# Performance work log

Hardware: AMD Instinct MI355X
Metric: run time of the kernel (lower is better)

The kernel has to match this reference:

```python
import jax, jax.numpy as jnp
import numpy as np

NH = 16   # num heads
CS = 16   # inner chunk size

def _gelu(x):
    return jax.nn.gelu(x, approximate=True)

def _diff_gelu(x):
    t = jnp.tanh(0.79788456 * x * (1.0 + 0.044715 * x * x))
    return 0.5 * x * ((1.0 - t * t) * (0.79788456 + 0.1070322243 * x * x)) + 0.5 * (1.0 + t)

def _ln_fused_l2_bwd(x, tgt, gamma, beta, eps=1e-6):
    # x, tgt: [B*nh, CS, f]; gamma/beta: [1, nh, 1, f]
    Bnh, N, HF = x.shape
    mu = x.mean(-1, keepdims=True)
    var = x.var(-1, keepdims=True)
    std = jnp.sqrt(var + eps)
    x_hat = (x - mu) / std
    y = gamma * x_hat.reshape(-1, NH, N, HF) + beta
    go = y - tgt.reshape(-1, NH, N, HF)
    gxh = (go * gamma).reshape(Bnh, N, HF)
    return (HF * gxh - gxh.sum(-1, keepdims=True) - x_hat * (gxh * x_hat).sum(-1, keepdims=True)) / (HF * std)

def setup_inputs() -> dict:
    key = jax.random.key(0)
    ks = jax.random.split(key, 8)
    B, nh, f, hf4, n_chunks = 4, NH, 64, 256, 128
    Bnh = B * nh
    XQ = jax.random.normal(ks[0], (n_chunks, Bnh, CS, f), jnp.float32)
    XK = jax.random.normal(ks[1], (n_chunks, Bnh, CS, f), jnp.float32)
    XV = jax.random.normal(ks[2], (n_chunks, Bnh, CS, f), jnp.float32)
    # inner-loop lr coeffs (ilr * token_idx ~ lr/head_dim): small positive
    coeff = jax.random.uniform(ks[3], (n_chunks, Bnh, CS, 1), jnp.float32) * 0.01
    coeff_last = jax.random.uniform(ks[4], (n_chunks, Bnh, 1, 1), jnp.float32) * 0.01
    W1 = jax.random.normal(ks[5], (Bnh, f, hf4), jnp.float32) * 0.02
    b1 = jnp.zeros((Bnh, 1, hf4), jnp.float32)
    W2 = jax.random.normal(ks[6], (Bnh, hf4, f), jnp.float32) * 0.02
    b2 = jnp.zeros((Bnh, 1, f), jnp.float32)
    ln_weight = jnp.ones((1, nh, 1, f), jnp.float32)
    ln_bias = jnp.zeros((1, nh, 1, f), jnp.float32)
    return dict(XQ=XQ, XK=XK, XV=XV, coeff=coeff, coeff_last=coeff_last,
                W1=W1, b1=b1, W2=W2, b2=b2, ln_weight=ln_weight, ln_bias=ln_bias)

def reference(XQ, XK, XV, coeff, coeff_last, W1, b1, W2, b2, ln_weight, ln_bias):
    n_chunks, Bnh, _, f = XQ.shape
    attn_b = jnp.tril(jnp.ones((CS, CS), XQ.dtype))

    def step(carry, inp):
        W1c, b1c, W2c, b2c = carry
        xv, xk, xq, c, cl = inp
        Z1 = xk @ W1c + b1c                      # [Bnh, CS, 4f]
        X2 = _gelu(Z1)
        Z2 = X2 @ W2c + b2c                      # [Bnh, CS, f]
        dZ2 = _ln_fused_l2_bwd(Z2, xv - xk, ln_weight, ln_bias)
        dZ1 = (dZ2 @ W2c.transpose(0, 2, 1)) * _diff_gelu(Z1)
        b1_bar = b1c - c * (attn_b @ dZ1)
        A1 = jnp.tril(xq @ xk.transpose(0, 2, 1))
        Z1_bar = xq @ W1c - c * (A1 @ dZ1) + b1_bar
        X2_bar = _gelu(Z1_bar)
        b2_bar = b2c - c * (attn_b @ dZ2)
        A2 = jnp.tril(X2_bar @ X2.transpose(0, 2, 1))
        Z2_bar = X2_bar @ W2c - c * (A2 @ dZ2) + b2_bar
        W1n = W1c - cl * (xk.transpose(0, 2, 1) @ dZ1)
        W2n = W2c - cl * (X2.transpose(0, 2, 1) @ dZ2)
        return (W1n, b1_bar[:, -1:], W2n, b2_bar[:, -1:]), Z2_bar

    _, Z2_all = jax.lax.scan(step, (W1, b1, W2, b2), (XV, XK, XQ, coeff, coeff_last))
    # [n_chunks, Bnh, CS, f] -> [Bnh, N, f]
    return Z2_all.transpose(1, 0, 2, 3).reshape(Bnh, n_chunks * CS, f)
```

## Files before the change

kernel.cpp:

```cpp
#include <hip/hip_runtime.h>

typedef __attribute__((ext_vector_type(8))) short bf16x8;
typedef __attribute__((ext_vector_type(4))) float f32x4;
typedef __attribute__((ext_vector_type(2))) unsigned int u32x2;

#define MFMA16(a,b,c) __builtin_amdgcn_mfma_f32_16x16x32_bf16(a,b,c,0,0,0)
#define A_GELU 0.7978845608028654f

#define OFF_W1B   0u
#define OFF_W2F   36864u
#define OFF_XK    70656u
#define OFF_XQ    72960u
#define OFF_X2    75264u
#define OFF_X2B   83712u
#define OFF_DZ2B  92160u
#define OFF_DZ1CT 94464u
#define OFF_DZ2CT 114944u
#define OFF_M1    120064u
#define OFF_M2    121344u
#define OFF_Z2F   122624u
#define OFF_Z2G   126976u
#define OFF_TGT   131328u
#define OFF_B2    135424u
#define OFF_COEF  135936u
#define OFF_CL    136000u
#define SMEM_BYTES 136016u

__device__ __forceinline__ float fast_tanh(float u){
    float e = __expf(2.0f*u);
    return 1.0f - 2.0f/(e + 1.0f);
}
__device__ __forceinline__ float gelu_f(float x){
    float t = fast_tanh(A_GELU*(x + 0.044715f*x*x*x));
    return 0.5f*x*(1.0f+t);
}
__device__ __forceinline__ float dgelu_f(float x){
    float x2 = x*x;
    float t = fast_tanh(A_GELU*x*(1.0f + 0.044715f*x2));
    return 0.5f*x*((1.0f-t*t)*(A_GELU + 0.1070322243f*x2)) + 0.5f*(1.0f+t);
}
__device__ __forceinline__ short f2bf(float f){
    unsigned u = __builtin_bit_cast(unsigned, f);
    u += 0x7FFFu + ((u >> 16) & 1u);
    return (short)(u >> 16);
}
__device__ __forceinline__ float bf2f(unsigned short s){
    unsigned u = ((unsigned)s) << 16;
    return __builtin_bit_cast(float, u);
}
__device__ __forceinline__ unsigned pkbf(float a, float b){
    unsigned r;
    asm("v_cvt_pk_bf16_f32 %0, %1, %2" : "=v"(r) : "v"(a), "v"(b));
    return r;
}
__device__ __forceinline__ bf16x8 ldfrag(const unsigned short* p){
    return *(const bf16x8*)p;
}

__global__ __launch_bounds__(512, 1)
void ttt_m2(const float* __restrict__ XQ, const float* __restrict__ XK,
            const float* __restrict__ XV, const float* __restrict__ coeff,
            const float* __restrict__ coeff_last,
            const float* __restrict__ W1g, const float* __restrict__ b1g,
            const float* __restrict__ W2g, const float* __restrict__ b2g,
            const float* __restrict__ gammag, const float* __restrict__ betag,
            float* __restrict__ out)
{
    const int h  = blockIdx.x;
    const int t  = threadIdx.x;
    const int l  = t & 63;
    const int w  = t >> 6;
    const int lo = l & 15;
    const int hi = l >> 4;

    extern __shared__ char smem[];
    unsigned short* sW1bu  = (unsigned short*)(smem + OFF_W1B);
    unsigned short* sW2fu  = (unsigned short*)(smem + OFF_W2F);
    unsigned short* sxku   = (unsigned short*)(smem + OFF_XK);
    unsigned short* sxqu   = (unsigned short*)(smem + OFF_XQ);
    unsigned short* sX2u   = (unsigned short*)(smem + OFF_X2);
    unsigned short* sX2bu  = (unsigned short*)(smem + OFF_X2B);
    unsigned short* sdZ2bu = (unsigned short*)(smem + OFF_DZ2B);
    unsigned short* sdZ1ct = (unsigned short*)(smem + OFF_DZ1CT);
    unsigned short* sdZ2ct = (unsigned short*)(smem + OFF_DZ2CT);
    unsigned short* sM1u   = (unsigned short*)(smem + OFF_M1);
    unsigned short* sM2u   = (unsigned short*)(smem + OFF_M2);
    float* sZ2f  = (float*)(smem + OFF_Z2F);
    float* sZ2g  = (float*)(smem + OFF_Z2G);
    float* stgt  = (float*)(smem + OFF_TGT);
    float* b2f   = (float*)(smem + OFF_B2);
    float* scoef = (float*)(smem + OFF_COEF);
    float* sCL   = (float*)(smem + OFF_CL);

    const int base1 = h*16384;
    const int base2 = h*16384;

    float mW1[4][2][4];
    float mW2[2][4][4];
    #pragma unroll
    for (int mt = 0; mt < 4; ++mt)
      #pragma unroll
      for (int tix = 0; tix < 2; ++tix)
        #pragma unroll
        for (int reg = 0; reg < 4; ++reg) {
            const int m = mt*16 + hi*4 + reg, n = (2*w + tix)*16 + lo;
            mW1[mt][tix][reg] = W1g[base1 + m*256 + n];
        }
    #pragma unroll
    for (int mi = 0; mi < 2; ++mi)
      #pragma unroll
      for (int nt = 0; nt < 4; ++nt)
        #pragma unroll
        for (int reg = 0; reg < 4; ++reg) {
            const int m = (2*w + mi)*16 + hi*4 + reg, n = nt*16 + lo;
            mW2[mi][nt][reg] = W2g[base2 + m*64 + n];
        }
    float b1reg[2];
    b1reg[0] = b1g[h*256 + (2*w)*16 + lo];
    b1reg[1] = b1g[h*256 + (2*w+1)*16 + lo];

    for (int i = 0; i < 32; ++i) {
        const int idx = i*512 + t;
        const int m = idx >> 8, n = idx & 255;
        sW1bu[n*72 + m] = f2bf(W1g[base1 + idx]);
    }
    for (int i = 0; i < 32; ++i) {
        const int idx = i*512 + t;
        const int hf = idx >> 6, f = idx & 63;
        sW2fu[f*264 + hf] = f2bf(W2g[base2 + idx]);
    }
    if (t < 64) b2f[t] = b2g[h*64 + t];
    if (t < 256) {
        for (int k = 16; k < 40; ++k) sdZ1ct[t*40 + k] = 0;
    }
    if (t < 64) {
        for (int k = 16; k < 40; ++k) sdZ2ct[t*40 + k] = 0;
    }
    if (t < 16) {
        for (int k = 16; k < 40; ++k) { sM1u[t*40 + k] = 0; sM2u[t*40 + k] = 0; }
    }

    const float gj = gammag[(h & 15)*64 + l];
    const float bj = betag [(h & 15)*64 + l];

    {
        const int r0 = w*2;
        const float xk0 = XK[h*1024 + r0*64 + l],     xq0 = XQ[h*1024 + r0*64 + l];
        const float xk1 = XK[h*1024 + (r0+1)*64 + l], xq1 = XQ[h*1024 + (r0+1)*64 + l];
        const float xv0 = XV[h*1024 + r0*64 + l],     xv1 = XV[h*1024 + (r0+1)*64 + l];
        const unsigned pkk = pkbf(xk0, xk1), pkq = pkbf(xq0, xq1);
        sxku[r0*72 + l]     = (unsigned short)pkk;
        sxku[(r0+1)*72 + l] = (unsigned short)(pkk >> 16);
        sxqu[r0*72 + l]     = (unsigned short)pkq;
        sxqu[(r0+1)*72 + l] = (unsigned short)(pkq >> 16);
        stgt[r0*64 + l]     = xv0 - xk0;
        stgt[(r0+1)*64 + l] = xv1 - xk1;
        if (t < 16)  scoef[t] = coeff[h*16 + t];
        if (t == 16) sCL[0]   = coeff_last[h];
    }
    __syncthreads();

    for (int ci = 0; ci < 128; ++ci) {
        const float clv = sCL[0];
        const float c15 = scoef[15];
        float crs[4];
        #pragma unroll
        for (int reg = 0; reg < 4; ++reg) crs[reg] = scoef[hi*4 + reg];

        float pxk[4], pxq[4], pxv[4];
        float pcf = 0.f, pcl = 0.f;
        if (w >= 4 && ci < 127) {
            const int cb1 = (ci + 1)*65536 + h*1024;
            const int r0 = (w - 4)*4;
            #pragma unroll
            for (int i = 0; i < 4; ++i) {
                pxk[i] = XK[cb1 + (r0 + i)*64 + l];
                pxq[i] = XQ[cb1 + (r0 + i)*64 + l];
                pxv[i] = XV[cb1 + (r0 + i)*64 + l];
            }
            const int u = t - 256;
            if (u < 16)  pcf = coeff[(ci + 1)*1024 + h*16 + u];
            if (u == 16) pcl = coeff_last[(ci + 1)*64 + h];
        }

        float z1s[8];
        bf16x8 afk0 = ldfrag(sxku + lo*72 + hi*8);
        bf16x8 afk1 = ldfrag(sxku + lo*72 + 32 + hi*8);
        #pragma unroll
        for (int tix = 0; tix < 2; ++tix) {
            const int n = (2*w + tix)*16 + lo;
            f32x4 acc = {b1reg[tix], b1reg[tix], b1reg[tix], b1reg[tix]};
            acc = MFMA16(afk0, ldfrag(sW1bu + n*72 + hi*8), acc);
            acc = MFMA16(afk1, ldfrag(sW1bu + n*72 + 32 + hi*8), acc);
            float g[4];
            #pragma unroll
            for (int reg = 0; reg < 4; ++reg) {
                z1s[tix*4 + reg] = acc[reg];
                g[reg] = gelu_f(acc[reg]);
            }
            const unsigned p01 = pkbf(g[0], g[1]), p23 = pkbf(g[2], g[3]);
            sX2u[(hi*4+0)*264 + n] = (unsigned short)p01;
            sX2u[(hi*4+1)*264 + n] = (unsigned short)(p01 >> 16);
            sX2u[(hi*4+2)*264 + n] = (unsigned short)p23;
            sX2u[(hi*4+3)*264 + n] = (unsigned short)(p23 >> 16);
        }
        if (w == 0) {
            bf16x8 aq0 = ldfrag(sxqu + lo*72 + hi*8);
            bf16x8 aq1 = ldfrag(sxqu + lo*72 + 32 + hi*8);
            f32x4 a1 = {0.f, 0.f, 0.f, 0.f};
            a1 = MFMA16(aq0, afk0, a1);
            a1 = MFMA16(aq1, afk1, a1);
            #pragma unroll
            for (int reg = 0; reg < 4; ++reg) {
                const int r = hi*4 + reg;
                const float v = (lo <= r) ? (-crs[reg]*(a1[reg] + 1.0f)) : 0.0f;
                sM1u[r*40 + lo] = f2bf(v);
            }
        }
        #pragma unroll
        for (int mi = 0; mi < 2; ++mi)
          #pragma unroll
          for (int nt = 0; nt < 4; ++nt) {
                const int n = nt*16 + lo, m0 = (2*w + mi)*16 + hi*4;
                *(u32x2*)&sW2fu[n*264 + m0] =
                    (u32x2){pkbf(mW2[mi][nt][0], mW2[mi][nt][1]),
                            pkbf(mW2[mi][nt][2], mW2[mi][nt][3])};
          }
        __syncthreads();

        const int tile = w & 3, kh = w >> 2;
        const int nf = tile*16 + lo;
        {
            f32x4 acc;
            if (kh == 0) {
                const float b2v = b2f[(ci & 1)*64 + nf];
                acc = (f32x4){b2v, b2v, b2v, b2v};
            } else acc = (f32x4){0.f, 0.f, 0.f, 0.f};
            #pragma unroll
            for (int s = 0; s < 4; ++s) {
                const int k = (kh*4 + s)*32 + hi*8;
                acc = MFMA16(ldfrag(sX2u + lo*264 + k),
                             ldfrag(sW2fu + nf*264 + k), acc);
            }
            float* dst = (kh == 0) ? sZ2g : sZ2f;
            #pragma unroll
            for (int reg = 0; reg < 4; ++reg)
                dst[(hi*4 + reg)*68 + nf] = acc[reg];
        }
        __syncthreads();

        {
            float dzp[2];
            #pragma unroll
            for (int i = 0; i < 2; ++i) {
                const int r = w*2 + i;
                const float z2 = sZ2f[r*68 + l] + sZ2g[r*68 + l];
                float s1 = z2, s2 = z2*z2;
                #pragma unroll
                for (int m = 1; m < 64; m <<= 1) { s1 += __shfl_xor(s1, m); s2 += __shfl_xor(s2, m); }
                const float mu   = s1*(1.0f/64.0f);
                const float var  = s2*(1.0f/64.0f) - mu*mu;
                const float rstd = rsqrtf(var + 1e-6f);
                const float xh   = (z2 - mu)*rstd;
                const float go   = gj*xh + bj - stgt[r*64 + l];
                const float gg   = go*gj;
                float u1 = gg, u2 = gg*xh;
                #pragma unroll
                for (int m = 1; m < 64; m <<= 1) { u1 += __shfl_xor(u1, m); u2 += __shfl_xor(u2, m); }
                dzp[i] = (64.0f*gg - u1 - xh*u2)*(rstd*(1.0f/64.0f));
            }
            const unsigned pk = pkbf(dzp[0], dzp[1]);
            sdZ2bu[(w*2)*72 + l]   = (unsigned short)pk;
            sdZ2bu[(w*2+1)*72 + l] = (unsigned short)(pk >> 16);
            *(unsigned*)&sdZ2ct[l*40 + w*2] = pk;
        }
        __syncthreads();

        float b1old[2];
        {
            bf16x8 ad0 = ldfrag(sdZ2bu + lo*72 + hi*8);
            bf16x8 ad1 = ldfrag(sdZ2bu + lo*72 + 32 + hi*8);
            #pragma unroll
            for (int tix = 0; tix < 2; ++tix) {
                const int n = (2*w + tix)*16 + lo;
                f32x4 acc = {0.f, 0.f, 0.f, 0.f};
                bf16x8 bw;
                #pragma unroll
                for (int j = 0; j < 8; ++j) bw[j] = (short)sW2fu[(hi*8 + j)*264 + n];
                acc = MFMA16(ad0, bw, acc);
                #pragma unroll
                for (int j = 0; j < 8; ++j) bw[j] = (short)sW2fu[(32 + hi*8 + j)*264 + n];
                acc = MFMA16(ad1, bw, acc);
                float dv[4], cs = 0.f;
                #pragma unroll
                for (int reg = 0; reg < 4; ++reg) {
                    dv[reg] = acc[reg]*dgelu_f(z1s[tix*4 + reg]);
                    cs += dv[reg];
                }
                *(u32x2*)&sdZ1ct[n*40 + hi*4] =
                    (u32x2){pkbf(dv[0], dv[1]), pkbf(dv[2], dv[3])};
                cs += __shfl_xor(cs, 16);
                cs += __shfl_xor(cs, 32);
                b1old[tix] = b1reg[tix];
                b1reg[tix] -= c15*cs;
            }
        }
        __syncthreads();

        {
            bf16x8 aq0 = ldfrag(sxqu + lo*72 + hi*8);
            bf16x8 aq1 = ldfrag(sxqu + lo*72 + 32 + hi*8);
            bf16x8 am1 = ldfrag(sM1u + lo*40 + hi*8);
            #pragma unroll
            for (int tix = 0; tix < 2; ++tix) {
                const int n = (2*w + tix)*16 + lo;
                f32x4 acc = {b1old[tix], b1old[tix], b1old[tix], b1old[tix]};
                acc = MFMA16(aq0, ldfrag(sW1bu + n*72 + hi*8), acc);
                acc = MFMA16(aq1, ldfrag(sW1bu + n*72 + 32 + hi*8), acc);
                acc = MFMA16(am1, ldfrag(sdZ1ct + n*40 + hi*8), acc);
                float g[4];
                #pragma unroll
                for (int reg = 0; reg < 4; ++reg) g[reg] = gelu_f(acc[reg]);
                const unsigned p01 = pkbf(g[0], g[1]), p23 = pkbf(g[2], g[3]);
                sX2bu[(hi*4+0)*264 + n] = (unsigned short)p01;
                sX2bu[(hi*4+1)*264 + n] = (unsigned short)(p01 >> 16);
                sX2bu[(hi*4+2)*264 + n] = (unsigned short)p23;
                sX2bu[(hi*4+3)*264 + n] = (unsigned short)(p23 >> 16);
            }
            bf16x8 bz0 = ldfrag(sdZ1ct + ((2*w)*16 + lo)*40 + hi*8);
            bf16x8 bz1 = ldfrag(sdZ1ct + ((2*w+1)*16 + lo)*40 + hi*8);
            #pragma unroll
            for (int mt = 0; mt < 4; ++mt) {
                bf16x8 axt = (bf16x8){0,0,0,0,0,0,0,0};
                if (l < 32) {
                    #pragma unroll
                    for (int j = 0; j < 8; ++j)
                        axt[j] = (short)sxku[(hi*8 + j)*72 + (mt*16 + lo)];
                }
                f32x4 z4 = {0.f,0.f,0.f,0.f};
                f32x4 u0 = MFMA16(axt, bz0, z4);
                f32x4 u1 = MFMA16(axt, bz1, z4);
                #pragma unroll
                for (int reg = 0; reg < 4; ++reg) {
                    mW1[mt][0][reg] -= clv*u0[reg];
                    mW1[mt][1][reg] -= clv*u1[reg];
                }
            }
        }
        __syncthreads();

        {
            bf16x8 bz2[4];
            #pragma unroll
            for (int nt = 0; nt < 4; ++nt)
                bz2[nt] = ldfrag(sdZ2ct + (nt*16 + lo)*40 + hi*8);
            #pragma unroll
            for (int mi = 0; mi < 2; ++mi) {
                const int mt = 2*w + mi;
                bf16x8 ax2 = (bf16x8){0,0,0,0,0,0,0,0};
                if (l < 32) {
                    #pragma unroll
                    for (int j = 0; j < 8; ++j)
                        ax2[j] = (short)sX2u[(hi*8 + j)*264 + (mt*16 + lo)];
                }
                #pragma unroll
                for (int nt = 0; nt < 4; ++nt) {
                    f32x4 z4 = {0.f,0.f,0.f,0.f};
                    f32x4 u = MFMA16(ax2, bz2[nt], z4);
                    #pragma unroll
                    for (int reg = 0; reg < 4; ++reg)
                        mW2[mi][nt][reg] -= clv*u[reg];
                }
            }
            if (w == 0) {
                f32x4 a2 = {0.f,0.f,0.f,0.f};
                #pragma unroll
                for (int ks = 0; ks < 8; ++ks) {
                    const int k = ks*32 + hi*8;
                    a2 = MFMA16(ldfrag(sX2bu + lo*264 + k),
                                ldfrag(sX2u + lo*264 + k), a2);
                }
                #pragma unroll
                for (int reg = 0; reg < 4; ++reg) {
                    const int r = hi*4 + reg;
                    const float v = (lo <= r) ? (-crs[reg]*(a2[reg] + 1.0f)) : 0.0f;
                    sM2u[r*40 + lo] = f2bf(v);
                }
            }
            if (w == 1) {
                float cs = 0.f;
                #pragma unroll
                for (int k = 0; k < 16; ++k) cs += bf2f(sdZ2ct[l*40 + k]);
                b2f[((ci + 1) & 1)*64 + l] = b2f[(ci & 1)*64 + l] - c15*cs;
            }
            #pragma unroll
            for (int mt = 0; mt < 4; ++mt)
              #pragma unroll
              for (int tix = 0; tix < 2; ++tix) {
                    const int n = (2*w + tix)*16 + lo, m0 = mt*16 + hi*4;
                    *(u32x2*)&sW1bu[n*72 + m0] =
                        (u32x2){pkbf(mW1[mt][tix][0], mW1[mt][tix][1]),
                                pkbf(mW1[mt][tix][2], mW1[mt][tix][3])};
              }
        }
        __syncthreads();

        if (w < 4) {
            const int nf2 = w*16 + lo;
            const float b2v = b2f[(ci & 1)*64 + nf2];
            f32x4 acc = {b2v, b2v, b2v, b2v};
            #pragma unroll
            for (int s = 0; s < 8; ++s) {
                const int k0 = s*32 + hi*8;
                acc = MFMA16(ldfrag(sX2bu + lo*264 + k0),
                             ldfrag(sW2fu + nf2*264 + k0), acc);
            }
            acc = MFMA16(ldfrag(sM2u + lo*40 + hi*8),
                         ldfrag(sdZ2ct + nf2*40 + hi*8), acc);
            #pragma unroll
            for (int reg = 0; reg < 4; ++reg)
                out[h*131072 + (ci*16 + hi*4 + reg)*64 + nf2] = acc[reg];
        } else if (ci < 127) {
            const int r0 = (w - 4)*4;
            #pragma unroll
            for (int p = 0; p < 2; ++p) {
                const int r = r0 + 2*p;
                const unsigned pkk = pkbf(pxk[2*p], pxk[2*p+1]);
                const unsigned pkq = pkbf(pxq[2*p], pxq[2*p+1]);
                sxku[r*72 + l]     = (unsigned short)pkk;
                sxku[(r+1)*72 + l] = (unsigned short)(pkk >> 16);
                sxqu[r*72 + l]     = (unsigned short)pkq;
                sxqu[(r+1)*72 + l] = (unsigned short)(pkq >> 16);
                stgt[r*64 + l]     = pxv[2*p]   - pxk[2*p];
                stgt[(r+1)*64 + l] = pxv[2*p+1] - pxk[2*p+1];
            }
            const int u = t - 256;
            if (u < 16)  scoef[u] = pcf;
            if (u == 16) sCL[0]   = pcl;
        }
        __syncthreads();
    }
}

extern "C" void kernel_launch(void* const* d_in, const int* in_sizes, int n_in,
                              void* d_out, int out_size, void* d_ws, size_t ws_size,
                              hipStream_t stream) {
    const float* XQ  = (const float*)d_in[0];
    const float* XK  = (const float*)d_in[1];
    const float* XV  = (const float*)d_in[2];
    const float* cf  = (const float*)d_in[3];
    const float* cfl = (const float*)d_in[4];
    const float* W1  = (const float*)d_in[5];
    const float* b1  = (const float*)d_in[6];
    const float* W2  = (const float*)d_in[7];
    const float* b2  = (const float*)d_in[8];
    const float* gam = (const float*)d_in[9];
    const float* bet = (const float*)d_in[10];
    float* o = (float*)d_out;

    hipFuncSetAttribute((const void*)ttt_m2,
                        hipFuncAttributeMaxDynamicSharedMemorySize, SMEM_BYTES);
    ttt_m2<<<64, 512, SMEM_BYTES, stream>>>(XQ, XK, XV, cf, cfl, W1, b1, W2, b2, gam, bet, o);
}
```

Before: 976.4 us.

## Add transposed W2 and XK LDS copies, shrink padded K-pad buffers

Keeps a second, transposed bf16 copy of W2 and of XK in shared memory so MFMA operand fragments come from one vector load each instead of eight strided scalar gathers. The K=16 buffers (dZ1, dZ2, M1, M2) now use a 24-element stride, and a masked fragment load zero-fills the upper K half instead of relying on zeroed padding. The target (XV-XK) is stored as bf16. The b2 column sum now reads from the row-major dZ2 buffer. Each step pays extra LDS writes to keep the transposed W2 copy current, and shared memory use grows, and the bf16 target loses precision in the LayerNorm gradient.

```diff
diff --git a/kernel.cpp b/kernel.cpp
--- a/kernel.cpp
+++ b/kernel.cpp
@@ -9,22 +9,24 @@
 
 #define OFF_W1B   0u
 #define OFF_W2F   36864u
-#define OFF_XK    70656u
-#define OFF_XQ    72960u
-#define OFF_X2    75264u
-#define OFF_X2B   83712u
-#define OFF_DZ2B  92160u
-#define OFF_DZ1CT 94464u
-#define OFF_DZ2CT 114944u
-#define OFF_M1    120064u
-#define OFF_M2    121344u
-#define OFF_Z2F   122624u
-#define OFF_Z2G   126976u
-#define OFF_TGT   131328u
-#define OFF_B2    135424u
-#define OFF_COEF  135936u
-#define OFF_CL    136000u
-#define SMEM_BYTES 136016u
+#define OFF_W2T   70656u
+#define OFF_XK    107520u
+#define OFF_XQ    109824u
+#define OFF_XKT   112128u
+#define OFF_X2    115200u
+#define OFF_X2B   123648u
+#define OFF_DZ2B  132096u
+#define OFF_DZ1CT 134400u
+#define OFF_DZ2CT 146688u
+#define OFF_M1    149760u
+#define OFF_M2    150528u
+#define OFF_Z2F   151296u
+#define OFF_Z2G   155520u
+#define OFF_TGT   159744u
+#define OFF_B2    162048u
+#define OFF_COEF  162560u
+#define OFF_CL    162624u
+#define SMEM_BYTES 162640u
 
 __device__ __forceinline__ float fast_tanh(float u){
     float e = __expf(2.0f*u);
@@ -55,6 +57,11 @@
 }
 __device__ __forceinline__ bf16x8 ldfrag(const unsigned short* p){
     return *(const bf16x8*)p;
+}
+__device__ __forceinline__ bf16x8 ldmask16(const unsigned short* row, int hi){
+    bf16x8 r = {0,0,0,0,0,0,0,0};
+    if (hi < 2) r = *(const bf16x8*)(row + hi*8);
+    return r;
 }
 
 __global__ __launch_bounds__(512, 1)
@@ -76,8 +83,10 @@
     extern __shared__ char smem[];
     unsigned short* sW1bu  = (unsigned short*)(smem + OFF_W1B);
     unsigned short* sW2fu  = (unsigned short*)(smem + OFF_W2F);
+    unsigned short* sW2T   = (unsigned short*)(smem + OFF_W2T);
     unsigned short* sxku   = (unsigned short*)(smem + OFF_XK);
     unsigned short* sxqu   = (unsigned short*)(smem + OFF_XQ);
+    unsigned short* sxkT   = (unsigned short*)(smem + OFF_XKT);
     unsigned short* sX2u   = (unsigned short*)(smem + OFF_X2);
     unsigned short* sX2bu  = (unsigned short*)(smem + OFF_X2B);
     unsigned short* sdZ2bu = (unsigned short*)(smem + OFF_DZ2B);
@@ -87,7 +96,7 @@
     unsigned short* sM2u   = (unsigned short*)(smem + OFF_M2);
     float* sZ2f  = (float*)(smem + OFF_Z2F);
     float* sZ2g  = (float*)(smem + OFF_Z2G);
-    float* stgt  = (float*)(smem + OFF_TGT);
+    unsigned short* stgtu = (unsigned short*)(smem + OFF_TGT);
     float* b2f   = (float*)(smem + OFF_B2);
     float* scoef = (float*)(smem + OFF_COEF);
     float* sCL   = (float*)(smem + OFF_CL);
@@ -127,18 +136,11 @@
     for (int i = 0; i < 32; ++i) {
         const int idx = i*512 + t;
         const int hf = idx >> 6, f = idx & 63;
-        sW2fu[f*264 + hf] = f2bf(W2g[base2 + idx]);
+        const short v = f2bf(W2g[base2 + idx]);
+        sW2fu[f*264 + hf] = v;
+        sW2T[hf*72 + f]   = v;
     }
     if (t < 64) b2f[t] = b2g[h*64 + t];
-    if (t < 256) {
-        for (int k = 16; k < 40; ++k) sdZ1ct[t*40 + k] = 0;
-    }
-    if (t < 64) {
-        for (int k = 16; k < 40; ++k) sdZ2ct[t*40 + k] = 0;
-    }
-    if (t < 16) {
-        for (int k = 16; k < 40; ++k) { sM1u[t*40 + k] = 0; sM2u[t*40 + k] = 0; }
-    }
 
     const float gj = gammag[(h & 15)*64 + l];
     const float bj = betag [(h & 15)*64 + l];
@@ -149,12 +151,14 @@
         const float xk1 = XK[h*1024 + (r0+1)*64 + l], xq1 = XQ[h*1024 + (r0+1)*64 + l];
         const float xv0 = XV[h*1024 + r0*64 + l],     xv1 = XV[h*1024 + (r0+1)*64 + l];
         const unsigned pkk = pkbf(xk0, xk1), pkq = pkbf(xq0, xq1);
+        const unsigned pkt = pkbf(xv0 - xk0, xv1 - xk1);
         sxku[r0*72 + l]     = (unsigned short)pkk;
         sxku[(r0+1)*72 + l] = (unsigned short)(pkk >> 16);
         sxqu[r0*72 + l]     = (unsigned short)pkq;
         sxqu[(r0+1)*72 + l] = (unsigned short)(pkq >> 16);
-        stgt[r0*64 + l]     = xv0 - xk0;
-        stgt[(r0+1)*64 + l] = xv1 - xk1;
+        *(unsigned*)&sxkT[l*24 + r0] = pkk;
+        stgtu[r0*72 + l]     = (unsigned short)pkt;
+        stgtu[(r0+1)*72 + l] = (unsigned short)(pkt >> 16);
         if (t < 16)  scoef[t] = coeff[h*16 + t];
         if (t == 16) sCL[0]   = coeff_last[h];
     }
@@ -214,7 +218,7 @@
             for (int reg = 0; reg < 4; ++reg) {
                 const int r = hi*4 + reg;
                 const float v = (lo <= r) ? (-crs[reg]*(a1[reg] + 1.0f)) : 0.0f;
-                sM1u[r*40 + lo] = f2bf(v);
+                sM1u[r*24 + lo] = f2bf(v);
             }
         }
         #pragma unroll
@@ -222,9 +226,13 @@
           #pragma unroll
           for (int nt = 0; nt < 4; ++nt) {
                 const int n = nt*16 + lo, m0 = (2*w + mi)*16 + hi*4;
-                *(u32x2*)&sW2fu[n*264 + m0] =
-                    (u32x2){pkbf(mW2[mi][nt][0], mW2[mi][nt][1]),
-                            pkbf(mW2[mi][nt][2], mW2[mi][nt][3])};
+                const unsigned p01 = pkbf(mW2[mi][nt][0], mW2[mi][nt][1]);
+                const unsigned p23 = pkbf(mW2[mi][nt][2], mW2[mi][nt][3]);
+                *(u32x2*)&sW2fu[n*264 + m0] = (u32x2){p01, p23};
+                sW2T[(m0+0)*72 + n] = (unsigned short)p01;
+                sW2T[(m0+1)*72 + n] = (unsigned short)(p01 >> 16);
+                sW2T[(m0+2)*72 + n] = (unsigned short)p23;
+                sW2T[(m0+3)*72 + n] = (unsigned short)(p23 >> 16);
           }
         __syncthreads();
 
@@ -245,7 +253,7 @@
             float* dst = (kh == 0) ? sZ2g : sZ2f;
             #pragma unroll
             for (int reg = 0; reg < 4; ++reg)
-                dst[(hi*4 + reg)*68 + nf] = acc[reg];
+                dst[(hi*4 + reg)*66 + nf] = acc[reg];
         }
         __syncthreads();
 
@@ -254,7 +262,7 @@
             #pragma unroll
             for (int i = 0; i < 2; ++i) {
                 const int r = w*2 + i;
-                const float z2 = sZ2f[r*68 + l] + sZ2g[r*68 + l];
+                const float z2 = sZ2f[r*66 + l] + sZ2g[r*66 + l];
                 float s1 = z2, s2 = z2*z2;
                 #pragma unroll
                 for (int m = 1; m < 64; m <<= 1) { s1 += __shfl_xor(s1, m); s2 += __shfl_xor(s2, m); }
@@ -262,7 +270,7 @@
                 const float var  = s2*(1.0f/64.0f) - mu*mu;
                 const float rstd = rsqrtf(var + 1e-6f);
                 const float xh   = (z2 - mu)*rstd;
-                const float go   = gj*xh + bj - stgt[r*64 + l];
+                const float go   = gj*xh + bj - bf2f(stgtu[r*72 + l]);
                 const float gg   = go*gj;
                 float u1 = gg, u2 = gg*xh;
                 #pragma unroll
@@ -272,7 +280,7 @@
             const unsigned pk = pkbf(dzp[0], dzp[1]);
             sdZ2bu[(w*2)*72 + l]   = (unsigned short)pk;
             sdZ2bu[(w*2+1)*72 + l] = (unsigned short)(pk >> 16);
-            *(unsigned*)&sdZ2ct[l*40 + w*2] = pk;
+            *(unsigned*)&sdZ2ct[l*24 + w*2] = pk;
         }
         __syncthreads();
 
@@ -284,20 +292,15 @@
             for (int tix = 0; tix < 2; ++tix) {
                 const int n = (2*w + tix)*16 + lo;
                 f32x4 acc = {0.f, 0.f, 0.f, 0.f};
-                bf16x8 bw;
-                #pragma unroll
-                for (int j = 0; j < 8; ++j) bw[j] = (short)sW2fu[(hi*8 + j)*264 + n];
-                acc = MFMA16(ad0, bw, acc);
-                #pragma unroll
-                for (int j = 0; j < 8; ++j) bw[j] = (short)sW2fu[(32 + hi*8 + j)*264 + n];
-                acc = MFMA16(ad1, bw, acc);
+                acc = MFMA16(ad0, ldfrag(sW2T + n*72 + hi*8), acc);
+                acc = MFMA16(ad1, ldfrag(sW2T + n*72 + 32 + hi*8), acc);
                 float dv[4], cs = 0.f;
                 #pragma unroll
                 for (int reg = 0; reg < 4; ++reg) {
                     dv[reg] = acc[reg]*dgelu_f(z1s[tix*4 + reg]);
                     cs += dv[reg];
                 }
-                *(u32x2*)&sdZ1ct[n*40 + hi*4] =
+                *(u32x2*)&sdZ1ct[n*24 + hi*4] =
                     (u32x2){pkbf(dv[0], dv[1]), pkbf(dv[2], dv[3])};
                 cs += __shfl_xor(cs, 16);
                 cs += __shfl_xor(cs, 32);
@@ -310,14 +313,14 @@
         {
             bf16x8 aq0 = ldfrag(sxqu + lo*72 + hi*8);
             bf16x8 aq1 = ldfrag(sxqu + lo*72 + 32 + hi*8);
-            bf16x8 am1 = ldfrag(sM1u + lo*40 + hi*8);
+            bf16x8 am1 = ldmask16(sM1u + lo*24, hi);
             #pragma unroll
             for (int tix = 0; tix < 2; ++tix) {
                 const int n = (2*w + tix)*16 + lo;
                 f32x4 acc = {b1old[tix], b1old[tix], b1old[tix], b1old[tix]};
                 acc = MFMA16(aq0, ldfrag(sW1bu + n*72 + hi*8), acc);
                 acc = MFMA16(aq1, ldfrag(sW1bu + n*72 + 32 + hi*8), acc);
-                acc = MFMA16(am1, ldfrag(sdZ1ct + n*40 + hi*8), acc);
+                acc = MFMA16(am1, ldmask16(sdZ1ct + n*24, hi), acc);
                 float g[4];
                 #pragma unroll
                 for (int reg = 0; reg < 4; ++reg) g[reg] = gelu_f(acc[reg]);
@@ -327,16 +330,11 @@
                 sX2bu[(hi*4+2)*264 + n] = (unsigned short)p23;
                 sX2bu[(hi*4+3)*264 + n] = (unsigned short)(p23 >> 16);
             }
-            bf16x8 bz0 = ldfrag(sdZ1ct + ((2*w)*16 + lo)*40 + hi*8);
-            bf16x8 bz1 = ldfrag(sdZ1ct + ((2*w+1)*16 + lo)*40 + hi*8);
+            bf16x8 bz0 = ldmask16(sdZ1ct + ((2*w)*16 + lo)*24, hi);
+            bf16x8 bz1 = ldmask16(sdZ1ct + ((2*w+1)*16 + lo)*24, hi);
             #pragma unroll
             for (int mt = 0; mt < 4; ++mt) {
-                bf16x8 axt = (bf16x8){0,0,0,0,0,0,0,0};
-                if (l < 32) {
-                    #pragma unroll
-                    for (int j = 0; j < 8; ++j)
-                        axt[j] = (short)sxku[(hi*8 + j)*72 + (mt*16 + lo)];
-                }
+                bf16x8 axt = ldmask16(sxkT + (mt*16 + lo)*24, hi);
                 f32x4 z4 = {0.f,0.f,0.f,0.f};
                 f32x4 u0 = MFMA16(axt, bz0, z4);
                 f32x4 u1 = MFMA16(axt, bz1, z4);
@@ -353,7 +351,7 @@
             bf16x8 bz2[4];
             #pragma unroll
             for (int nt = 0; nt < 4; ++nt)
-                bz2[nt] = ldfrag(sdZ2ct + (nt*16 + lo)*40 + hi*8);
+                bz2[nt] = ldmask16(sdZ2ct + (nt*16 + lo)*24, hi);
             #pragma unroll
             for (int mi = 0; mi < 2; ++mi) {
                 const int mt = 2*w + mi;
@@ -384,13 +382,13 @@
                 for (int reg = 0; reg < 4; ++reg) {
                     const int r = hi*4 + reg;
                     const float v = (lo <= r) ? (-crs[reg]*(a2[reg] + 1.0f)) : 0.0f;
-                    sM2u[r*40 + lo] = f2bf(v);
+                    sM2u[r*24 + lo] = f2bf(v);
                 }
             }
             if (w == 1) {
                 float cs = 0.f;
                 #pragma unroll
-                for (int k = 0; k < 16; ++k) cs += bf2f(sdZ2ct[l*40 + k]);
+                for (int k = 0; k < 16; ++k) cs += bf2f(sdZ2bu[k*72 + l]);
                 b2f[((ci + 1) & 1)*64 + l] = b2f[(ci & 1)*64 + l] - c15*cs;
             }
             #pragma unroll
@@ -415,8 +413,8 @@
                 acc = MFMA16(ldfrag(sX2bu + lo*264 + k0),
                              ldfrag(sW2fu + nf2*264 + k0), acc);
             }
-            acc = MFMA16(ldfrag(sM2u + lo*40 + hi*8),
-                         ldfrag(sdZ2ct + nf2*40 + hi*8), acc);
+            acc = MFMA16(ldmask16(sM2u + lo*24, hi),
+                         ldmask16(sdZ2ct + nf2*24, hi), acc);
             #pragma unroll
             for (int reg = 0; reg < 4; ++reg)
                 out[h*131072 + (ci*16 + hi*4 + reg)*64 + nf2] = acc[reg];
@@ -427,12 +425,14 @@
                 const int r = r0 + 2*p;
                 const unsigned pkk = pkbf(pxk[2*p], pxk[2*p+1]);
                 const unsigned pkq = pkbf(pxq[2*p], pxq[2*p+1]);
+                const unsigned pkt = pkbf(pxv[2*p] - pxk[2*p], pxv[2*p+1] - pxk[2*p+1]);
                 sxku[r*72 + l]     = (unsigned short)pkk;
                 sxku[(r+1)*72 + l] = (unsigned short)(pkk >> 16);
                 sxqu[r*72 + l]     = (unsigned short)pkq;
                 sxqu[(r+1)*72 + l] = (unsigned short)(pkq >> 16);
-                stgt[r*64 + l]     = pxv[2*p]   - pxk[2*p];
-                stgt[(r+1)*64 + l] = pxv[2*p+1] - pxk[2*p+1];
+                *(unsigned*)&sxkT[l*24 + r] = pkk;
+                stgtu[r*72 + l]     = (unsigned short)pkt;
+                stgtu[(r+1)*72 + l] = (unsigned short)(pkt >> 16);
             }
             const int u = t - 256;
             if (u < 16)  scoef[u] = pcf;
```

After: 866.9 us. 1.13x faster.
